# Performance work log

Hardware: AMD Instinct MI355X
Metric: run time of the kernel (lower is better)

Reference implementation:

```python
import jax, jax.numpy as jnp
import numpy as np

N, E, D, G, NTYPES = 50000, 400000, 64, 512, 64


def _bn(x, g, b):
    # BatchNorm1d in training mode: biased batch stats, eps=1e-5, affine g/b
    mu = x.mean(0)
    var = ((x - mu) ** 2).mean(0)
    return g * (x - mu) * jax.lax.rsqrt(var + 1e-5) + b


def _rotmat(a):
    t, p, q = a[0], a[1], a[2]
    ct, st = jnp.cos(t), jnp.sin(t)
    cp, sp = jnp.cos(p), jnp.sin(p)
    cq, sq = jnp.cos(q), jnp.sin(q)
    z = jnp.zeros(())
    o = jnp.ones(())
    Rt = jnp.array([[ct, -st, z], [st, ct, z], [z, z, o]])
    Rp = jnp.array([[cp, z, -sp], [z, o, z], [sp, z, cp]])
    Rq = jnp.array([[o, z, z], [z, cq, -sq], [z, sq, cq]])
    return Rt @ Rp @ Rq


def _egat(src, dst, nf, ef, Wnode, bnode, Wni, Wnj, Wfij, attn, H):
    # DGL EGATConv: edge feats from src/dst node + edge projections, edge-softmax attention over dst
    n = nf.shape[0]
    f_out = jax.nn.leaky_relu((nf @ Wni)[src] + (nf @ Wnj)[dst] + ef @ Wfij)  # [E, H*D]
    f_out = f_out.reshape(-1, H, D)
    e = (f_out * attn[None]).sum(-1)  # [E, H]
    emax = jax.ops.segment_max(e, dst, num_segments=n)
    ee = jnp.exp(e - emax[dst])
    a = ee / jax.ops.segment_sum(ee, dst, num_segments=n)[dst]
    hsrc = (nf @ Wnode + bnode).reshape(n, H, D)[src]
    h_out = jax.ops.segment_sum(hsrc * a[:, :, None], dst, num_segments=n)  # [N, H, D]
    return h_out, f_out


def _layer(src, dst, nh, eh, p, H, last):
    Wnode, bnode, Wni, Wnj, Wfij, attn, bnn_g, bnn_b, bne_g, bne_b, Wpn, bpn, Wpe, bpe = p
    hn, he = _egat(src, dst, nh, eh, Wnode, bnode, Wni, Wnj, Wfij, attn, H)
    if last:
        hn, he = hn.mean(1), he.mean(1)
    else:
        hn, he = hn.reshape(hn.shape[0], -1), he.reshape(he.shape[0], -1)
    hn = _bn(hn, bnn_g, bnn_b)
    he = _bn(he, bne_g, bne_b)
    return hn @ Wpn + bpn + nh, he @ Wpe + bpe + eh


def setup_inputs():
    key = jax.random.key(0)
    kit = iter(jax.random.split(key, 64))

    def rn(shape, s=0.05):
        return jax.random.normal(next(kit), shape, dtype=jnp.float32) * s

    inp = {}
    inp["ntype"] = jax.random.randint(next(kit), (N, 1), 0, NTYPES)
    inp["src"] = jax.random.randint(next(kit), (E,), 0, N)
    inp["dst"] = jax.random.randint(next(kit), (E,), 0, N)
    inp["graph_ids"] = jnp.sort(jax.random.randint(next(kit), (N,), 0, G))
    inp["angles_rot"] = rn((3,), 1.0)
    inp["angles_ref"] = rn((3,), 1.0)
    inp["efeats"] = rn((E, 3), 1.0)
    inp["emb_table"] = rn((NTYPES, D))
    inp["enc_W"] = rn((D, D)); inp["enc_b"] = jnp.zeros((D,))
    inp["ee_W1"] = rn((3, D)); inp["ee_b1"] = jnp.zeros((D,))
    inp["ee_W2"] = rn((D, D)); inp["ee_b2"] = jnp.zeros((D,))
    for nm in ["enc_bn1", "enc_bn2", "ee_bn1", "ee_bn2"]:
        inp[nm + "_g"] = jnp.ones((D,)); inp[nm + "_b"] = jnp.zeros((D,))
    for l, H in [(0, 2), (1, 1)]:
        p = "l%d_" % l
        inp[p + "Wnode"] = rn((D, H * D)); inp[p + "bnode"] = jnp.zeros((H * D,))
        inp[p + "Wni"] = rn((D, H * D)); inp[p + "Wnj"] = rn((D, H * D)); inp[p + "Wfij"] = rn((D, H * D))
        inp[p + "attn"] = rn((H, D))
        inp[p + "bnn_g"] = jnp.ones((H * D,)); inp[p + "bnn_b"] = jnp.zeros((H * D,))
        inp[p + "bne_g"] = jnp.ones((H * D,)); inp[p + "bne_b"] = jnp.zeros((H * D,))
        inp[p + "Wpn"] = rn((H * D, D)); inp[p + "bpn"] = jnp.zeros((D,))
        inp[p + "Wpe"] = rn((H * D, D)); inp[p + "bpe"] = jnp.zeros((D,))
    inp["dec_W"] = rn((4, D, D)); inp["dec_b"] = jnp.zeros((4, D))
    inp["dec_bn_g"] = jnp.ones((4, D)); inp["dec_bn_b"] = jnp.zeros((4, D))
    inp["dec_prelu"] = jnp.full((4,), 0.25, dtype=jnp.float32)
    inp["dec_Wout"] = rn((D, 1)); inp["dec_bout"] = jnp.zeros((1,))
    return inp


def reference(efeats, emb_table, enc_bn1_g, enc_bn1_b, enc_W, enc_b, enc_bn2_g, enc_bn2_b, ee_W1, ee_b1, ee_bn1_g, ee_bn1_b, ee_W2, ee_b2, ee_bn2_g, ee_bn2_b, l0_Wnode, l0_bnode, l0_Wni, l0_Wnj, l0_Wfij, l0_attn, l0_bnn_g, l0_bnn_b, l0_bne_g, l0_bne_b, l0_Wpn, l0_bpn, l0_Wpe, l0_bpe, l1_Wnode, l1_bnode, l1_Wni, l1_Wnj, l1_Wfij, l1_attn, l1_bnn_g, l1_bnn_b, l1_bne_g, l1_bne_b, l1_Wpn, l1_bpn, l1_Wpe, l1_bpe, dec_W, dec_b, dec_bn_g, dec_bn_b, dec_prelu, dec_Wout, dec_bout, ntype, src, dst, graph_ids, angles_rot, angles_ref):
    # node encoder: Embedding -> BN -> ReLU -> Linear -> BN -> ReLU
    nh = emb_table[ntype[:, 0]]
    nh = jax.nn.relu(_bn(nh, enc_bn1_g, enc_bn1_b))
    nh = jax.nn.relu(_bn(nh @ enc_W + enc_b, enc_bn2_g, enc_bn2_b))

    def edge_enc(f):
        h = jax.nn.relu(_bn(f @ ee_W1 + ee_b1, ee_bn1_g, ee_bn1_b))
        return jax.nn.relu(_bn(h @ ee_W2 + ee_b2, ee_bn2_g, ee_bn2_b))

    # rotation matrices built from sampled angles; torch.tensor([...]) detaches -> stop_gradient
    R_rot = jax.lax.stop_gradient(_rotmat(angles_rot))
    R_ref = -jax.lax.stop_gradient(_rotmat(angles_ref))
    eh = edge_enc(efeats @ R_rot) + edge_enc(efeats @ R_ref)

    p0 = (l0_Wnode, l0_bnode, l0_Wni, l0_Wnj, l0_Wfij, l0_attn, l0_bnn_g, l0_bnn_b, l0_bne_g, l0_bne_b, l0_Wpn, l0_bpn, l0_Wpe, l0_bpe)
    p1 = (l1_Wnode, l1_bnode, l1_Wni, l1_Wnj, l1_Wfij, l1_attn, l1_bnn_g, l1_bnn_b, l1_bne_g, l1_bne_b, l1_Wpn, l1_bpn, l1_Wpe, l1_bpe)
    nh, eh = _layer(src, dst, nh, eh, p0, 2, False)
    h1 = nh
    nh, eh = _layer(src, dst, nh, eh, p1, 1, True)
    h2 = nh

    h = nh
    for i in range(4):
        h = _bn(h @ dec_W[i] + dec_b[i], dec_bn_g[i], dec_bn_b[i])
        h = jnp.where(h >= 0.0, h, dec_prelu[i] * h)
    h = h @ dec_Wout + dec_bout
    # dgl.sum_nodes: per-graph sum over batched graphs
    return (h1, h2, jax.ops.segment_sum(h, graph_ids, num_segments=G))
```

## Files before the change

### kernel.cpp

```cpp
#include <hip/hip_runtime.h>
#include <math.h>

#define NN 50000
#define NE 400000
#define NG 512
#define EPS 1e-5f
#define NSLOT 256

typedef unsigned int u32;
typedef unsigned short u16;

typedef __attribute__((ext_vector_type(8))) short s16x8;
typedef __attribute__((ext_vector_type(4))) float f32x4;

__device__ __forceinline__ float b2f(u16 h) { return __uint_as_float(((u32)h) << 16); }
__device__ __forceinline__ u16 f2b(float f) {
    u32 x = __float_as_uint(f);
    u32 r = x + 0x7fffu + ((x >> 16) & 1u);
    return (u16)(r >> 16);
}
struct alignas(16) U16x8 { u16 s[8]; };
struct alignas(8) U16x4 { u16 s[4]; };
struct alignas(4) U16x2 { u16 s[2]; };

__device__ __forceinline__ void f4add(float4& a, const float4 b) {
    a.x += b.x; a.y += b.y; a.z += b.z; a.w += b.w;
}

__device__ __forceinline__ int xcd_swizzle(int orig, int nwg) {
    int xcd = orig & 7;
    int q = nwg >> 3, r = nwg & 7;
    return (xcd < r ? xcd * (q + 1) : r * (q + 1) + (xcd - r) * q) + (orig >> 3);
}

__global__ void setup_kernel(const float* __restrict__ ang_rot, const float* __restrict__ ang_ref,
                             const float* __restrict__ W1, float* __restrict__ RWrot,
                             float* __restrict__ RWref) {
    int c = threadIdx.x;
    for (int which = 0; which < 2; ++which) {
        const float* a = which ? ang_ref : ang_rot;
        float t = a[0], p = a[1], q = a[2];
        float ct = cosf(t), st = sinf(t);
        float cp = cosf(p), sp = sinf(p);
        float cq = cosf(q), sq = sinf(q);
        float Rt[3][3] = {{ct, -st, 0.f}, {st, ct, 0.f}, {0.f, 0.f, 1.f}};
        float Rp[3][3] = {{cp, 0.f, -sp}, {0.f, 1.f, 0.f}, {sp, 0.f, cp}};
        float Rq[3][3] = {{1.f, 0.f, 0.f}, {0.f, cq, -sq}, {0.f, sq, cq}};
        float Rtp[3][3], R[3][3];
        for (int i = 0; i < 3; ++i)
            for (int j = 0; j < 3; ++j) {
                float s = 0.f;
                for (int k = 0; k < 3; ++k) s += Rt[i][k] * Rp[k][j];
                Rtp[i][j] = s;
            }
        for (int i = 0; i < 3; ++i)
            for (int j = 0; j < 3; ++j) {
                float s = 0.f;
                for (int k = 0; k < 3; ++k) s += Rtp[i][k] * Rq[k][j];
                R[i][j] = s;
            }
        float sgn = which ? -1.f : 1.f;
        float* RW = which ? RWref : RWrot;
        if (c < 64) {
            for (int j = 0; j < 3; ++j) {
                float s = 0.f;
                for (int m = 0; m < 3; ++m) s += sgn * R[j][m] * W1[m * 64 + c];
                RW[j * 64 + c] = s;
            }
        }
    }
}

#define NWT 17
struct WtJobs {
    const float* W[NWT];
    u16* WT[NWT];
    int K[NWT];
    int C[NWT];
};
__global__ __launch_bounds__(256) void wt_all_kernel(WtJobs jobs) {
    int job = blockIdx.x >> 5;
    int idx = ((blockIdx.x & 31) << 8) + threadIdx.x;
    int K = jobs.K[job], C = jobs.C[job];
    if (idx >= K * C) return;
    int k = idx / C, c = idx - k * C;
    jobs.WT[job][c * K + k] = f2b(jobs.W[job][idx]);
}

__global__ __launch_bounds__(256) void hist_kernel(const int* __restrict__ dst, int E,
                                                   int* __restrict__ deg) {
    int e = blockIdx.x * 256 + threadIdx.x;
    if (e < E) atomicAdd(&deg[dst[e]], 1);
}

__global__ __launch_bounds__(256) void scan_part_kernel(const int* __restrict__ deg,
                                                        int* __restrict__ bsum, int n) {
    int i = blockIdx.x * 256 + threadIdx.x;
    int v = (i < n) ? deg[i] : 0;
#pragma unroll
    for (int off = 1; off < 64; off <<= 1) v += __shfl_xor(v, off, 64);
    __shared__ int ws[4];
    if ((threadIdx.x & 63) == 0) ws[threadIdx.x >> 6] = v;
    __syncthreads();
    if (threadIdx.x == 0) bsum[blockIdx.x] = ws[0] + ws[1] + ws[2] + ws[3];
}

__global__ __launch_bounds__(256) void scan_top_kernel(int* __restrict__ bsum, int nb,
                                                       int* __restrict__ rowptr, int n,
                                                       int total) {
    __shared__ int s[256];
    int tid = threadIdx.x;
    s[tid] = (tid < nb) ? bsum[tid] : 0;
    __syncthreads();
    for (int off = 1; off < 256; off <<= 1) {
        int v = (tid >= off) ? s[tid - off] : 0;
        __syncthreads();
        s[tid] += v;
        __syncthreads();
    }
    if (tid < nb) bsum[tid] = (tid == 0) ? 0 : s[tid - 1];
    if (tid == 0) rowptr[n] = total;
}

__global__ __launch_bounds__(256) void scan_fill_kernel(const int* __restrict__ deg,
                                                        const int* __restrict__ bsum,
                                                        int* __restrict__ rowptr,
                                                        int* __restrict__ curs, int n) {
    __shared__ int s[256];
    int tid = threadIdx.x;
    int i = blockIdx.x * 256 + tid;
    int v = (i < n) ? deg[i] : 0;
    s[tid] = v;
    __syncthreads();
    for (int off = 1; off < 256; off <<= 1) {
        int t = (tid >= off) ? s[tid - off] : 0;
        __syncthreads();
        s[tid] += t;
        __syncthreads();
    }
    if (i < n) {
        int excl = s[tid] - v + bsum[blockIdx.x];
        rowptr[i] = excl;
        curs[i] = excl;
    }
}

__global__ __launch_bounds__(256) void fill_kernel(const int* __restrict__ src,
                                                   const int* __restrict__ dst,
                                                   const float* __restrict__ ef, int E,
                                                   int* __restrict__ curs,
                                                   int* __restrict__ esrc,
                                                   int* __restrict__ dsts,
                                                   float* __restrict__ efp) {
    int e = blockIdx.x * 256 + threadIdx.x;
    if (e >= E) return;
    int d = dst[e];
    int pos = atomicAdd(&curs[d], 1);
    esrc[pos] = src[e];
    dsts[pos] = d;
    efp[(long)pos * 3 + 0] = ef[(long)e * 3 + 0];
    efp[(long)pos * 3 + 1] = ef[(long)e * 3 + 1];
    efp[(long)pos * 3 + 2] = ef[(long)e * 3 + 2];
}

__global__ __launch_bounds__(256) void gather_emb_kernel(const int* __restrict__ ntype,
                                                         const float* __restrict__ emb,
                                                         u16* __restrict__ out, int n) {
    long i = (long)blockIdx.x * 256 + threadIdx.x;
    long e = i >> 3;
    if (e >= n) return;
    int c0 = (int)(i & 7) * 8;
    int t = ntype[e];
    float4 a = *(const float4*)&emb[(long)t * 64 + c0];
    float4 b = *(const float4*)&emb[(long)t * 64 + c0 + 4];
    U16x8 o;
    o.s[0] = f2b(a.x); o.s[1] = f2b(a.y); o.s[2] = f2b(a.z); o.s[3] = f2b(a.w);
    o.s[4] = f2b(b.x); o.s[5] = f2b(b.y); o.s[6] = f2b(b.z); o.s[7] = f2b(b.w);
    *(U16x8*)&out[e * 64 + c0] = o;
}

__global__ __launch_bounds__(256) void efstats_kernel(const float* __restrict__ ef, int E,
                                                      float* __restrict__ raw) {
    int tid = threadIdx.x;
    float a[9];
#pragma unroll
    for (int j = 0; j < 9; ++j) a[j] = 0.f;
    for (long e = (long)blockIdx.x * 256 + tid; e < E; e += (long)gridDim.x * 256) {
        float f0 = ef[e * 3 + 0], f1 = ef[e * 3 + 1], f2 = ef[e * 3 + 2];
        a[0] += f0; a[1] += f1; a[2] += f2;
        a[3] += f0 * f0; a[4] += f1 * f1; a[5] += f2 * f2;
        a[6] += f0 * f1; a[7] += f0 * f2; a[8] += f1 * f2;
    }
#pragma unroll
    for (int off = 1; off < 64; off <<= 1)
#pragma unroll
        for (int j = 0; j < 9; ++j) a[j] += __shfl_xor(a[j], off, 64);
    __shared__ float sred[4][9];
    int wv = tid >> 6, ln = tid & 63;
    if (ln == 0)
#pragma unroll
        for (int j = 0; j < 9; ++j) sred[wv][j] = a[j];
    __syncthreads();
    if (tid < 9) {
        float v = sred[0][tid] + sred[1][tid] + sred[2][tid] + sred[3][tid];
        atomicAdd(&raw[(size_t)(blockIdx.x & (NSLOT - 1)) * 16 + tid], v);
    }
}

__global__ void ee_stats_kernel(const float* __restrict__ efraw, const float* __restrict__ RWrot,
                                const float* __restrict__ RWref, const float* __restrict__ b1,
                                float* __restrict__ S_rot, float* __restrict__ S_ref, int E) {
    __shared__ float m[9];
    int t = threadIdx.x;
    if (t < 9) {
        float s = 0.f;
        for (int r = 0; r < NSLOT; ++r) s += efraw[r * 16 + t];
        m[t] = s;
    }
    __syncthreads();
    int br = t >> 6, c = t & 63;
    const float* RW = br ? RWref : RWrot;
    float* S = br ? S_ref : S_rot;
    float w0 = RW[c], w1 = RW[64 + c], w2 = RW[128 + c];
    float bb = b1[c];
    float mw = m[0] * w0 + m[1] * w1 + m[2] * w2;
    float sum = mw + (float)E * bb;
    float quad = m[3] * w0 * w0 + m[4] * w1 * w1 + m[5] * w2 * w2 +
                 2.f * (m[6] * w0 * w1 + m[7] * w0 * w2 + m[8] * w1 * w2);
    float ss = quad + 2.f * bb * mw + (float)E * bb * bb;
    S[c] = sum;
    S[64 + c] = ss;
}

template <int COLS>
__global__ __launch_bounds__(256) void colstats_kernel(const u16* __restrict__ xv, int rows,
                                                       float* __restrict__ raw) {
    constexpr int TPR = COLS / 8;
    constexpr int RPB = 256 / TPR;
    __shared__ float4 sA[256], sB[256], sC[256], sD[256];
    int tid = threadIdx.x;
    int c8 = tid % TPR;
    int rl = tid / TPR;
    float s[8], q[8];
#pragma unroll
    for (int j = 0; j < 8; ++j) { s[j] = 0.f; q[j] = 0.f; }
    const long stride = (long)gridDim.x * RPB;
    for (long r = (long)blockIdx.x * RPB + rl; r < rows; r += stride) {
        U16x8 t = *(const U16x8*)&xv[r * COLS + c8 * 8];
#pragma unroll
        for (int j = 0; j < 8; ++j) {
            float v = b2f(t.s[j]);
            s[j] += v;
            q[j] += v * v;
        }
    }
    sA[tid] = make_float4(s[0], s[1], s[2], s[3]);
    sB[tid] = make_float4(s[4], s[5], s[6], s[7]);
    sC[tid] = make_float4(q[0], q[1], q[2], q[3]);
    sD[tid] = make_float4(q[4], q[5], q[6], q[7]);
    __syncthreads();
    for (int off = 128; off >= TPR; off >>= 1) {
        if (tid < off) {
            f4add(sA[tid], sA[tid + off]); f4add(sB[tid], sB[tid + off]);
            f4add(sC[tid], sC[tid + off]); f4add(sD[tid], sD[tid + off]);
        }
        __syncthreads();
    }
    if (tid < TPR) {
        float* slot = raw + (size_t)(blockIdx.x & (NSLOT - 1)) * 256;
        int c = tid * 8;
        float4 a = sA[tid], b = sB[tid], cq = sC[tid], d = sD[tid];
        atomicAdd(&slot[c + 0], a.x); atomicAdd(&slot[c + 1], a.y);
        atomicAdd(&slot[c + 2], a.z); atomicAdd(&slot[c + 3], a.w);
        atomicAdd(&slot[c + 4], b.x); atomicAdd(&slot[c + 5], b.y);
        atomicAdd(&slot[c + 6], b.z); atomicAdd(&slot[c + 7], b.w);
        atomicAdd(&slot[COLS + c + 0], cq.x); atomicAdd(&slot[COLS + c + 1], cq.y);
        atomicAdd(&slot[COLS + c + 2], cq.z); atomicAdd(&slot[COLS + c + 3], cq.w);
        atomicAdd(&slot[COLS + c + 4], d.x); atomicAdd(&slot[COLS + c + 5], d.y);
        atomicAdd(&slot[COLS + c + 6], d.z); atomicAdd(&slot[COLS + c + 7], d.w);
    }
}

__global__ __launch_bounds__(256) void finalize_stats_kernel(const float* __restrict__ raw,
                                                             float* __restrict__ stats, int n) {
    int i = threadIdx.x;
    if (i >= n) return;
    float s = 0.f;
    for (int r = 0; r < NSLOT; ++r) s += raw[r * 256 + i];
    stats[i] = s;
}

__global__ __launch_bounds__(256) void bn_act_kernel(const u16* __restrict__ x,
                                                     u16* __restrict__ y, long rows, int cols,
                                                     const float* __restrict__ acc,
                                                     const float* __restrict__ g,
                                                     const float* __restrict__ b,
                                                     float inv_rows) {
    long i = (long)blockIdx.x * 256 + threadIdx.x;
    long total8 = rows * (long)cols / 8;
    if (i >= total8) return;
    long base = i * 8;
    int c0 = (int)(base % cols);
    U16x8 xv = *(const U16x8*)&x[base];
    U16x8 o;
#pragma unroll
    for (int j = 0; j < 8; ++j) {
        int c = c0 + j;
        float mu = acc[c] * inv_rows;
        float var = acc[cols + c] * inv_rows - mu * mu;
        float al = g[c] * rsqrtf(fmaxf(var, 0.f) + EPS);
        float be = b[c] - mu * al;
        o.s[j] = f2b(fmaxf(al * b2f(xv.s[j]) + be, 0.f));
    }
    *(U16x8*)&y[base] = o;
}


template <int K, int COLS, bool XBF, bool RBF, bool OBF, bool SOUT>
__global__ __launch_bounds__(256) void mfma_mm_kernel(
    const void* __restrict__ Xv, const u16* __restrict__ WT, const float* __restrict__ bias,
    const void* __restrict__ resv, void* __restrict__ Yv, int rows, int preop,
    const float* __restrict__ stats, const float* __restrict__ g, const float* __restrict__ b,
    float inv_rows, const float* __restrict__ prelu, int prelu_idx, float* __restrict__ raw) {
    constexpr int NCT = COLS / 16;
    constexpr int NKK = K / 32;
    __shared__ float al[K], be[K];
    __shared__ float ssum[SOUT ? COLS : 1], ssq[SOUT ? COLS : 1];
    const int tid = threadIdx.x;
    if (preop) {
        for (int k = tid; k < K; k += 256) {
            float mu = stats[k] * inv_rows;
            float var = stats[K + k] * inv_rows - mu * mu;
            float a = g[k] * rsqrtf(fmaxf(var, 0.f) + EPS);
            al[k] = a;
            be[k] = b[k] - mu * a;
        }
    }
    if (SOUT) {
        for (int i = tid; i < COLS; i += 256) { ssum[i] = 0.f; ssq[i] = 0.f; }
    }
    __syncthreads();
    const int lane = tid & 63, wv = tid >> 6;
    const int q = lane >> 4, rr = lane & 15;
    const long r0 = ((long)blockIdx.x * 4 + wv) * 16;
    const bool act = r0 < rows;
    const float pa = (preop == 3) ? prelu[prelu_idx] : 0.f;
    s16x8 afr[NKK];
    if (act) {
#pragma unroll
        for (int kk = 0; kk < NKK; ++kk) {
            float v[8];
            if (XBF) {
                U16x8 t = *(const U16x8*)((const u16*)Xv + (r0 + rr) * K + kk * 32 + q * 8);
#pragma unroll
                for (int j = 0; j < 8; ++j) v[j] = b2f(t.s[j]);
            } else {
                const float* xp = (const float*)Xv + (r0 + rr) * K + kk * 32 + q * 8;
                float4 t0 = *(const float4*)xp;
                float4 t1 = *(const float4*)(xp + 4);
                v[0] = t0.x; v[1] = t0.y; v[2] = t0.z; v[3] = t0.w;
                v[4] = t1.x; v[5] = t1.y; v[6] = t1.z; v[7] = t1.w;
            }
            union { u16 u[8]; s16x8 s; } o;
#pragma unroll
            for (int j = 0; j < 8; ++j) {
                float xx = v[j];
                if (preop) {
                    int k = kk * 32 + q * 8 + j;
                    xx = al[k] * xx + be[k];
                    if (preop == 2) xx = fmaxf(xx, 0.f);
                    else if (preop == 3) xx = (xx >= 0.f) ? xx : pa * xx;
                }
                o.u[j] = f2b(xx);
            }
            afr[kk] = o.s;
        }
#pragma unroll
        for (int ct = 0; ct < NCT; ++ct) {
            f32x4 acc = (f32x4){0.f, 0.f, 0.f, 0.f};
#pragma unroll
            for (int kk = 0; kk < NKK; ++kk) {
                s16x8 bfr = *(const s16x8*)&WT[(size_t)(ct * 16 + rr) * K + kk * 32 + q * 8];
                acc = __builtin_amdgcn_mfma_f32_16x16x32_bf16(afr[kk], bfr, acc, 0, 0, 0);
            }
            int col = ct * 16 + rr;
            float bb = bias ? bias[col] : 0.f;
            float fs = 0.f, fq = 0.f;
#pragma unroll
            for (int r = 0; r < 4; ++r) {
                long orr = r0 + q * 4 + r;
                float vv = acc[r] + bb;
                if (resv) {
                    if (RBF) vv += b2f(((const u16*)resv)[orr * COLS + col]);
                    else vv += ((const float*)resv)[orr * COLS + col];
                }
                if (OBF) ((u16*)Yv)[orr * COLS + col] = f2b(vv);
                else ((float*)Yv)[orr * COLS + col] = vv;
                if (SOUT) { fs += vv; fq += vv * vv; }
            }
            if (SOUT) {
                fs += __shfl_xor(fs, 16, 64); fs += __shfl_xor(fs, 32, 64);
                fq += __shfl_xor(fq, 16, 64); fq += __shfl_xor(fq, 32, 64);
                if (q == 0) {
                    atomicAdd(&ssum[col], fs);
                    atomicAdd(&ssq[col], fq);
                }
            }
        }
    }
    if (SOUT) {
        __syncthreads();
        float* slot = raw + (size_t)(blockIdx.x & (NSLOT - 1)) * 256;
        for (int i = tid; i < COLS; i += 256) {
            atomicAdd(&slot[i], ssum[i]);
            atomicAdd(&slot[COLS + i], ssq[i]);
        }
    }
}

template <int COLS, bool XBF>
__global__ __launch_bounds__(256) void mfma_mm3_kernel(
    const void* __restrict__ Xv, const u16* __restrict__ WT0, const u16* __restrict__ WT1,
    const u16* __restrict__ WT2, const float* __restrict__ bias2, u16* __restrict__ Y0,
    u16* __restrict__ Y1, u16* __restrict__ Y2, int rows) {
    constexpr int NCT = COLS / 16;
    const int tid = threadIdx.x;
    const int lane = tid & 63, wv = tid >> 6;
    const int q = lane >> 4, rr = lane & 15;
    const long r0 = ((long)blockIdx.x * 4 + wv) * 16;
    if (r0 >= rows) return;
    s16x8 afr[2];
#pragma unroll
    for (int kk = 0; kk < 2; ++kk) {
        if (XBF) {
            afr[kk] = *(const s16x8*)((const u16*)Xv + (r0 + rr) * 64 + kk * 32 + q * 8);
        } else {
            const float* xp = (const float*)Xv + (r0 + rr) * 64 + kk * 32 + q * 8;
            float4 t0 = *(const float4*)xp;
            float4 t1 = *(const float4*)(xp + 4);
            union { u16 u[8]; s16x8 s; } o;
            o.u[0] = f2b(t0.x); o.u[1] = f2b(t0.y); o.u[2] = f2b(t0.z); o.u[3] = f2b(t0.w);
            o.u[4] = f2b(t1.x); o.u[5] = f2b(t1.y); o.u[6] = f2b(t1.z); o.u[7] = f2b(t1.w);
            afr[kk] = o.s;
        }
    }
    const u16* wts[3] = {WT0, WT1, WT2};
    u16* ys[3] = {Y0, Y1, Y2};
#pragma unroll
    for (int m = 0; m < 3; ++m) {
#pragma unroll
        for (int ct = 0; ct < NCT; ++ct) {
            f32x4 acc = (f32x4){0.f, 0.f, 0.f, 0.f};
#pragma unroll
            for (int kk = 0; kk < 2; ++kk) {
                s16x8 bfr = *(const s16x8*)&wts[m][(size_t)(ct * 16 + rr) * 64 + kk * 32 + q * 8];
                acc = __builtin_amdgcn_mfma_f32_16x16x32_bf16(afr[kk], bfr, acc, 0, 0, 0);
            }
            int col = ct * 16 + rr;
            float bb = (m == 2) ? bias2[col] : 0.f;
#pragma unroll
            for (int r = 0; r < 4; ++r) {
                long orr = r0 + q * 4 + r;
                ys[m][orr * COLS + col] = f2b(acc[r] + bb);
            }
        }
    }
}

template <bool STORE>
__global__ __launch_bounds__(256) void mfma_ee2_kernel(
    const float* __restrict__ efp, const float* __restrict__ RWrot,
    const float* __restrict__ RWref, const float* __restrict__ b1v, const u16* __restrict__ W2T,
    const float* __restrict__ b2, const float* __restrict__ S1r, const float* __restrict__ S1f,
    const float* __restrict__ S2r, const float* __restrict__ S2f, const float* __restrict__ g1,
    const float* __restrict__ bn1b, const float* __restrict__ g2, const float* __restrict__ bn2b,
    u16* __restrict__ EH, int E, float inv_rows, float* __restrict__ rawA,
    float* __restrict__ rawB) {
    constexpr int ESTR = 72;
    __shared__ float rws[2][192];
    __shared__ float al1[2][64], be1[2][64];
    __shared__ float al2[2][64], be2[2][64];
    __shared__ float ssum[2][64], ssq[2][64];
    __shared__ u16 ets[STORE ? 64 * ESTR : 1];
    const int tid = threadIdx.x;
    if (tid < 192) {
        rws[0][tid] = RWrot[tid];
        rws[1][tid] = RWref[tid];
    }
    if (tid < 128) {
        int br = tid >> 6, k = tid & 63;
        const float* S1 = br ? S1f : S1r;
        float mu = S1[k] * inv_rows;
        float var = S1[64 + k] * inv_rows - mu * mu;
        float a = g1[k] * rsqrtf(fmaxf(var, 0.f) + EPS);
        al1[br][k] = a;
        be1[br][k] = bn1b[k] - mu * a + a * b1v[k];
        if (STORE) {
            const float* S2 = br ? S2f : S2r;
            mu = S2[k] * inv_rows;
            var = S2[64 + k] * inv_rows - mu * mu;
            a = g2[k] * rsqrtf(fmaxf(var, 0.f) + EPS);
            al2[br][k] = a;
            be2[br][k] = bn2b[k] - mu * a + a * b2[k];
        } else {
            ssum[br][k] = 0.f;
            ssq[br][k] = 0.f;
        }
    }
    __syncthreads();
    const int lane = tid & 63, wv = tid >> 6;
    const int q = lane >> 4, rr = lane & 15;
    const long r0 = ((long)blockIdx.x * 4 + wv) * 16;
    const long ar = r0 + rr;
    float e0 = efp[ar * 3], e1 = efp[ar * 3 + 1], e2 = efp[ar * 3 + 2];
    float v0[4][4];
#pragma unroll
    for (int br = 0; br < 2; ++br) {
        s16x8 afr[2];
#pragma unroll
        for (int kk = 0; kk < 2; ++kk) {
            union { u16 u[8]; s16x8 v; } t;
#pragma unroll
            for (int j = 0; j < 8; ++j) {
                int k = kk * 32 + q * 8 + j;
                float tv = e0 * rws[br][k] + e1 * rws[br][64 + k] + e2 * rws[br][128 + k];
                t.u[j] = f2b(fmaxf(al1[br][k] * tv + be1[br][k], 0.f));
            }
            afr[kk] = t.v;
        }
#pragma unroll
        for (int ct = 0; ct < 4; ++ct) {
            f32x4 acc = (f32x4){0.f, 0.f, 0.f, 0.f};
#pragma unroll
            for (int kk = 0; kk < 2; ++kk) {
                s16x8 bfr = *(const s16x8*)&W2T[(size_t)(ct * 16 + rr) * 64 + kk * 32 + q * 8];
                acc = __builtin_amdgcn_mfma_f32_16x16x32_bf16(afr[kk], bfr, acc, 0, 0, 0);
            }
            int col = ct * 16 + rr;
            if (STORE) {
#pragma unroll
                for (int r = 0; r < 4; ++r) {
                    float v = fmaxf(al2[br][col] * acc[r] + be2[br][col], 0.f);
                    if (br == 0) {
                        v0[ct][r] = v;
                    } else {
                        ets[(wv * 16 + q * 4 + r) * ESTR + col] = f2b(v0[ct][r] + v);
                    }
                }
            } else {
                float bb = b2[col];
                float s = 0.f, qq = 0.f;
#pragma unroll
                for (int r = 0; r < 4; ++r) {
                    float v = acc[r] + bb;
                    s += v;
                    qq += v * v;
                }
                s += __shfl_xor(s, 16, 64); s += __shfl_xor(s, 32, 64);
                qq += __shfl_xor(qq, 16, 64); qq += __shfl_xor(qq, 32, 64);
                if (q == 0) {
                    atomicAdd(&ssum[br][col], s);
                    atomicAdd(&ssq[br][col], qq);
                }
            }
        }
    }
    __syncthreads();
    if (STORE) {
        const long rb = (long)blockIdx.x * 64;
        for (int i = tid; i < 64 * 8; i += 256) {
            int row = i >> 3, c8 = i & 7;
            U16x8 v = *(const U16x8*)&ets[row * ESTR + c8 * 8];
            *(U16x8*)&EH[(rb + row) * 64 + c8 * 8] = v;
        }
    } else {
        if (tid < 128) {
            int br = tid >> 6, k = tid & 63;
            float* slot = (br ? rawB : rawA) + (size_t)(blockIdx.x & (NSLOT - 1)) * 256;
            atomicAdd(&slot[k], ssum[br][k]);
            atomicAdd(&slot[64 + k], ssq[br][k]);
        }
    }
}

template <int COLS, bool WRITE_F, bool SOUT>
__global__ __launch_bounds__(256) void mfma_egat_kernel(
    const u16* __restrict__ EH, const u16* __restrict__ WT, const u16* __restrict__ NI,
    const u16* __restrict__ NJ, const int* __restrict__ srcs, const int* __restrict__ dsts,
    const float* __restrict__ attn, u16* __restrict__ Fout, float* __restrict__ eatt, int E,
    float* __restrict__ raw) {
    constexpr int H = COLS / 64;
    constexpr int NCT = COLS / 16;
    constexpr int FSTR = COLS + 8;
    __shared__ float ssum[SOUT ? COLS : 1];
    __shared__ float ssq[SOUT ? COLS : 1];
    __shared__ u16 fts[WRITE_F ? 64 * FSTR : 1];
    const int tid = threadIdx.x;
    if (SOUT) {
        for (int i = tid; i < COLS; i += 256) { ssum[i] = 0.f; ssq[i] = 0.f; }
        __syncthreads();
    }
    const int bid = xcd_swizzle(blockIdx.x, gridDim.x);
    const int lane = tid & 63, wv = tid >> 6;
    const int q = lane >> 4, rr = lane & 15;
    const long r0 = ((long)bid * 4 + wv) * 16;
    s16x8 afr[2];
#pragma unroll
    for (int kk = 0; kk < 2; ++kk)
        afr[kk] = *(const s16x8*)&EH[(r0 + rr) * 64 + kk * 32 + q * 8];
    int sidx[4], didx[4];
#pragma unroll
    for (int r = 0; r < 4; ++r) {
        long orr = r0 + q * 4 + r;
        sidx[r] = srcs[orr];
        didx[r] = dsts[orr];
    }
    f32x4 acc[NCT];
#pragma unroll
    for (int ct = 0; ct < NCT; ++ct) {
        acc[ct] = (f32x4){0.f, 0.f, 0.f, 0.f};
#pragma unroll
        for (int kk = 0; kk < 2; ++kk) {
            s16x8 bfr = *(const s16x8*)&WT[(size_t)(ct * 16 + rr) * 64 + kk * 32 + q * 8];
            acc[ct] = __builtin_amdgcn_mfma_f32_16x16x32_bf16(afr[kk], bfr, acc[ct], 0, 0, 0);
        }
    }
    float part[H][4];
#pragma unroll
    for (int h = 0; h < H; ++h)
#pragma unroll
        for (int r = 0; r < 4; ++r) part[h][r] = 0.f;
#pragma unroll
    for (int ct = 0; ct < NCT; ++ct) {
        int col = ct * 16 + rr;
        float av = attn[col];
        const int h = (H == 2) ? (ct >> 2) : 0;
        float fs = 0.f, fq = 0.f;
#pragma unroll
        for (int r = 0; r < 4; ++r) {
            float f = acc[ct][r] + b2f(NI[(size_t)sidx[r] * COLS + col]) +
                      b2f(NJ[(size_t)didx[r] * COLS + col]);
            f = (f >= 0.f) ? f : 0.01f * f;
            if (WRITE_F) fts[(wv * 16 + q * 4 + r) * FSTR + col] = f2b(f);
            part[h][r] += f * av;
            if (SOUT) { fs += f; fq += f * f; }
        }
        if (SOUT) {
            fs += __shfl_xor(fs, 16, 64); fs += __shfl_xor(fs, 32, 64);
            fq += __shfl_xor(fq, 16, 64); fq += __shfl_xor(fq, 32, 64);
            if (q == 0) {
                atomicAdd(&ssum[col], fs);
                atomicAdd(&ssq[col], fq);
            }
        }
    }
#pragma unroll
    for (int h = 0; h < H; ++h)
#pragma unroll
        for (int r = 0; r < 4; ++r) {
            float p = part[h][r];
            p += __shfl_xor(p, 1, 64);
            p += __shfl_xor(p, 2, 64);
            p += __shfl_xor(p, 4, 64);
            p += __shfl_xor(p, 8, 64);
            part[h][r] = p;
        }
    if (rr == 0) {
#pragma unroll
        for (int r = 0; r < 4; ++r) {
            long pos = r0 + q * 4 + r;
            if (H == 2) {
                eatt[pos * 2 + 0] = part[0][r];
                eatt[pos * 2 + 1] = part[1][r];
            } else {
                eatt[pos] = part[0][r];
            }
        }
    }
    if (WRITE_F) {
        __syncthreads();
        const long rb = (long)bid * 64;
        constexpr int CH = COLS / 8;
        for (int i = tid; i < 64 * CH; i += 256) {
            int row = i / CH, c8 = i % CH;
            U16x8 v = *(const U16x8*)&fts[row * FSTR + c8 * 8];
            *(U16x8*)&Fout[(rb + row) * COLS + c8 * 8] = v;
        }
    }
    if (SOUT) {
        __syncthreads();
        float* slot = raw + (size_t)(blockIdx.x & (NSLOT - 1)) * 256;
        for (int i = tid; i < COLS; i += 256) {
            atomicAdd(&slot[i], ssum[i]);
            atomicAdd(&slot[COLS + i], ssq[i]);
        }
    }
}

__global__ __launch_bounds__(256) void mfma_pe_kernel(
    const u16* __restrict__ X, const u16* __restrict__ WT, const float* __restrict__ bias,
    u16* __restrict__ EHio, int E, const float* __restrict__ stats, const float* __restrict__ g,
    const float* __restrict__ b, float inv_rows) {
    constexpr int ESTR = 72;
    __shared__ float al[128], be[128];
    __shared__ u16 ets[64 * ESTR];
    const int tid = threadIdx.x;
    if (tid < 128) {
        float mu = stats[tid] * inv_rows;
        float var = stats[128 + tid] * inv_rows - mu * mu;
        float a = g[tid] * rsqrtf(fmaxf(var, 0.f) + EPS);
        al[tid] = a;
        be[tid] = b[tid] - mu * a;
    }
    __syncthreads();
    const int lane = tid & 63, wv = tid >> 6;
    const int q = lane >> 4, rr = lane & 15;
    const long r0 = ((long)blockIdx.x * 4 + wv) * 16;
    s16x8 afr[4];
#pragma unroll
    for (int kk = 0; kk < 4; ++kk) {
        U16x8 t = *(const U16x8*)&X[(r0 + rr) * 128 + kk * 32 + q * 8];
        union { u16 u[8]; s16x8 v; } o;
#pragma unroll
        for (int j = 0; j < 8; ++j) {
            int k = kk * 32 + q * 8 + j;
            o.u[j] = f2b(al[k] * b2f(t.s[j]) + be[k]);
        }
        afr[kk] = o.v;
    }
#pragma unroll
    for (int ct = 0; ct < 4; ++ct) {
        f32x4 acc = (f32x4){0.f, 0.f, 0.f, 0.f};
#pragma unroll
        for (int kk = 0; kk < 4; ++kk) {
            s16x8 bfr = *(const s16x8*)&WT[(size_t)(ct * 16 + rr) * 128 + kk * 32 + q * 8];
            acc = __builtin_amdgcn_mfma_f32_16x16x32_bf16(afr[kk], bfr, acc, 0, 0, 0);
        }
        int col = ct * 16 + rr;
        float bb = bias[col];
#pragma unroll
        for (int r = 0; r < 4; ++r)
            ets[(wv * 16 + q * 4 + r) * ESTR + col] = f2b(acc[r] + bb);
    }
    __syncthreads();
    const long rb = (long)blockIdx.x * 64;
#pragma unroll
    for (int g2 = 0; g2 < 2; ++g2) {
        int i = g2 * 256 + tid;
        int row = i >> 3, c8 = i & 7;
        U16x8 st = *(const U16x8*)&ets[row * ESTR + c8 * 8];
        U16x8 old = *(const U16x8*)&EHio[(rb + row) * 64 + c8 * 8];
        U16x8 o;
#pragma unroll
        for (int j = 0; j < 8; ++j) o.s[j] = f2b(b2f(st.s[j]) + b2f(old.s[j]));
        *(U16x8*)&EHio[(rb + row) * 64 + c8 * 8] = o;
    }
}

template <int COLS, bool SOUT>
__global__ __launch_bounds__(256) void csr_aggregate_kernel(
    const int* __restrict__ rowptr, const int* __restrict__ esrc,
    const float* __restrict__ eatt, const u16* __restrict__ nodeh, float* __restrict__ hout,
    int n, float* __restrict__ raw) {
    constexpr int H = COLS / 64;
    constexpr int TPN = COLS / 2;
    constexpr int NPB = 256 / TPN;
    __shared__ float ssum[SOUT ? COLS : 1];
    __shared__ float ssq[SOUT ? COLS : 1];
    int tid = threadIdx.x;
    if (SOUT) {
        for (int i = tid; i < COLS; i += 256) { ssum[i] = 0.f; ssq[i] = 0.f; }
        __syncthreads();
    }
    int node = blockIdx.x * NPB + tid / TPN;
    bool act = node < n;
    int c = (tid % TPN) * 2;
    float a0 = 0.f, a1 = 0.f;
    if (act) {
        int h = (H == 2) ? (c >> 6) : 0;
        int p0 = rowptr[node], p1 = rowptr[node + 1];
        float m = -INFINITY, s = 0.f;
        for (int p = p0; p < p1; ++p) {
            float v = eatt[(long)p * H + h];
            float mn = fmaxf(m, v);
            s = s * expf(m - mn) + expf(v - mn);
            m = mn;
        }
        float inv = (s > 0.f) ? 1.f / s : 0.f;
        for (int p = p0; p < p1; ++p) {
            float w = expf(eatt[(long)p * H + h] - m) * inv;
            U16x2 v = *(const U16x2*)&nodeh[(long)esrc[p] * COLS + c];
            a0 += b2f(v.s[0]) * w;
            a1 += b2f(v.s[1]) * w;
        }
        *(float2*)&hout[(long)node * COLS + c] = make_float2(a0, a1);
    }
    if (SOUT) {
        if (act) {
            atomicAdd(&ssum[c], a0);
            atomicAdd(&ssum[c + 1], a1);
            atomicAdd(&ssq[c], a0 * a0);
            atomicAdd(&ssq[c + 1], a1 * a1);
        }
        __syncthreads();
        float* slot = raw + (size_t)(blockIdx.x & (NSLOT - 1)) * 256;
        for (int i = tid; i < COLS; i += 256) {
            atomicAdd(&slot[i], ssum[i]);
            atomicAdd(&slot[COLS + i], ssq[i]);
        }
    }
}

__global__ __launch_bounds__(256) void decoder_out_kernel(
    const u16* __restrict__ t3, const float* __restrict__ stats, const float* __restrict__ g,
    const float* __restrict__ b, const float* __restrict__ prelu, const float* __restrict__ Wout,
    const float* __restrict__ bout, const int* __restrict__ gid, float* __restrict__ pool,
    int rows, float inv_rows) {
    int tid = threadIdx.x;
    long r = (long)blockIdx.x * 4 + (tid >> 6);
    if (r >= rows) return;
    int k = tid & 63;
    float mu = stats[k] * inv_rows;
    float var = stats[64 + k] * inv_rows - mu * mu;
    float al = g[k] * rsqrtf(fmaxf(var, 0.f) + EPS);
    float be = b[k] - mu * al;
    float a = prelu[3];
    float v = al * b2f(t3[r * 64 + k]) + be;
    v = (v >= 0.f) ? v : a * v;
    v *= Wout[k];
#pragma unroll
    for (int off = 1; off < 64; off <<= 1) v += __shfl_xor(v, off, 64);
    if (k == 0) atomicAdd(&pool[gid[r]], v + bout[0]);
}

extern "C" void kernel_launch(void* const* d_in, const int* in_sizes, int n_in, void* d_out,
                              int out_size, void* d_ws, size_t ws_size, hipStream_t stream) {
    if (n_in < 57) return;
    const int* ntype = (const int*)d_in[0];
    const int* src = (const int*)d_in[1];
    const int* dst = (const int*)d_in[2];
    const int* gid = (const int*)d_in[3];
    const float* ang_rot = (const float*)d_in[4];
    const float* ang_ref = (const float*)d_in[5];
    const float* efeats = (const float*)d_in[6];
    const float* emb = (const float*)d_in[7];
    const float* enc_W = (const float*)d_in[8];
    const float* enc_b = (const float*)d_in[9];
    const float* ee_W1 = (const float*)d_in[10];
    const float* ee_b1 = (const float*)d_in[11];
    const float* ee_W2 = (const float*)d_in[12];
    const float* ee_b2 = (const float*)d_in[13];
    const float* enc_bn1_g = (const float*)d_in[14];
    const float* enc_bn1_b = (const float*)d_in[15];
    const float* enc_bn2_g = (const float*)d_in[16];
    const float* enc_bn2_b = (const float*)d_in[17];
    const float* ee_bn1_g = (const float*)d_in[18];
    const float* ee_bn1_b = (const float*)d_in[19];
    const float* ee_bn2_g = (const float*)d_in[20];
    const float* ee_bn2_b = (const float*)d_in[21];
    const float* l0_Wnode = (const float*)d_in[22];
    const float* l0_bnode = (const float*)d_in[23];
    const float* l0_Wni = (const float*)d_in[24];
    const float* l0_Wnj = (const float*)d_in[25];
    const float* l0_Wfij = (const float*)d_in[26];
    const float* l0_attn = (const float*)d_in[27];
    const float* l0_bnn_g = (const float*)d_in[28];
    const float* l0_bnn_b = (const float*)d_in[29];
    const float* l0_bne_g = (const float*)d_in[30];
    const float* l0_bne_b = (const float*)d_in[31];
    const float* l0_Wpn = (const float*)d_in[32];
    const float* l0_bpn = (const float*)d_in[33];
    const float* l0_Wpe = (const float*)d_in[34];
    const float* l0_bpe = (const float*)d_in[35];
    const float* l1_Wnode = (const float*)d_in[36];
    const float* l1_bnode = (const float*)d_in[37];
    const float* l1_Wni = (const float*)d_in[38];
    const float* l1_Wnj = (const float*)d_in[39];
    const float* l1_Wfij = (const float*)d_in[40];
    const float* l1_attn = (const float*)d_in[41];
    const float* l1_bnn_g = (const float*)d_in[42];
    const float* l1_bnn_b = (const float*)d_in[43];
    const float* l1_Wpn = (const float*)d_in[46];
    const float* l1_bpn = (const float*)d_in[47];
    const float* dec_W = (const float*)d_in[50];
    const float* dec_b = (const float*)d_in[51];
    const float* dec_bn_g = (const float*)d_in[52];
    const float* dec_bn_b = (const float*)d_in[53];
    const float* dec_prelu = (const float*)d_in[54];
    const float* dec_Wout = (const float*)d_in[55];
    const float* dec_bout = (const float*)d_in[56];

    float* out = (float*)d_out;
    float* H1 = out;
    float* H2 = out + (long)NN * 64;
    float* POOL = out + (long)NN * 128;

    char* base = (char*)d_ws;
    size_t off = 0;
    auto alloc = [&](size_t bytes) -> void* {
        off = (off + 255) & ~(size_t)255;
        void* p = base + off;
        off += bytes;
        return p;
    };
    u16* EH = (u16*)alloc((size_t)NE * 64 * 2);
    u16* F128 = (u16*)alloc((size_t)NE * 128 * 2);
    float* EATT = (float*)alloc((size_t)NE * 2 * 4);
    u16* NX = (u16*)alloc((size_t)NN * 64 * 2);
    u16* NI = (u16*)alloc((size_t)NN * 128 * 2);
    u16* NJ = (u16*)alloc((size_t)NN * 128 * 2);
    u16* NHH = (u16*)alloc((size_t)NN * 128 * 2);
    float* HOUT0 = (float*)alloc((size_t)NN * 128 * 4);
    float* HOUT1 = (float*)alloc((size_t)NN * 64 * 4);
    int* ROWPTR = (int*)alloc((size_t)(NN + 1) * 4);
    int* CURS = (int*)alloc((size_t)NN * 4);
    int* ESRC = (int*)alloc((size_t)NE * 4);
    int* DSTS = (int*)alloc((size_t)NE * 4);
    float* EFP = (float*)alloc((size_t)NE * 3 * 4);
    int* BSUM = (int*)alloc((size_t)256 * 4);
    float* RWrot = (float*)alloc(256 * 4);
    float* RWref = (float*)alloc(256 * 4);
    u16* EncWT = (u16*)alloc(4096 * 2);
    u16* W2T = (u16*)alloc(4096 * 2);
    u16* Wni0T = (u16*)alloc(8192 * 2);
    u16* Wnj0T = (u16*)alloc(8192 * 2);
    u16* Wnd0T = (u16*)alloc(8192 * 2);
    u16* WfijT0 = (u16*)alloc(8192 * 2);
    u16* Wpn0T = (u16*)alloc(8192 * 2);
    u16* WpeT = (u16*)alloc(8192 * 2);
    u16* Wni1T = (u16*)alloc(4096 * 2);
    u16* Wnj1T = (u16*)alloc(4096 * 2);
    u16* Wnd1T = (u16*)alloc(4096 * 2);
    u16* WfijT1 = (u16*)alloc(4096 * 2);
    u16* Wpn1T = (u16*)alloc(4096 * 2);
    u16* DecT0 = (u16*)alloc(4096 * 2);
    u16* DecT1 = (u16*)alloc(4096 * 2);
    u16* DecT2 = (u16*)alloc(4096 * 2);
    u16* DecT3 = (u16*)alloc(4096 * 2);
    float* STATS = (float*)alloc((size_t)13 * 256 * 4);
    char* zstart = base + ((off + 255) & ~(size_t)255);
    int* DEG = (int*)alloc((size_t)NN * 4);
    float* STATS_RAW = (float*)alloc((size_t)13 * NSLOT * 256 * 4);
    float* RAWEF = (float*)alloc((size_t)NSLOT * 16 * 4);
    char* zend = base + off;
    if (ws_size < off) return;

    u16* NX0 = F128;
    u16* NT = F128 + (size_t)NN * 64;
    u16* DT0 = NI;
    u16* DT1 = NJ;

    auto RAW = [&](int idx) { return STATS_RAW + (size_t)idx * NSLOT * 256; };
    float* S_enc1 = STATS + 0 * 256;
    float* S_enc2 = STATS + 1 * 256;
    float* S_ee1r = STATS + 2 * 256;
    float* S_ee2r = STATS + 3 * 256;
    float* S_ee1f = STATS + 4 * 256;
    float* S_ee2f = STATS + 5 * 256;
    float* S_bnn0 = STATS + 6 * 256;
    float* S_bne0 = STATS + 7 * 256;
    float* S_bnn1 = STATS + 8 * 256;
    float* S_d0 = STATS + 9 * 256;
    float* S_d1 = STATS + 10 * 256;
    float* S_d2 = STATS + 11 * 256;
    float* S_d3 = STATS + 12 * 256;

    const float invN = 1.f / (float)NN;
    const float invE = 1.f / (float)NE;
    const int GS = 640;
    const int MFB = NE / 64;
    const int NNB = (NN + 63) / 64;
    const int NB = (NN + 255) / 256;

    hipMemsetAsync(zstart, 0, (size_t)(zend - zstart), stream);
    hipMemsetAsync(POOL, 0, (size_t)NG * 4, stream);

    setup_kernel<<<1, 64, 0, stream>>>(ang_rot, ang_ref, ee_W1, RWrot, RWref);
    {
        WtJobs j;
        const float* Ws[NWT] = {enc_W,  ee_W2,  l0_Wni, l0_Wnj, l0_Wnode, l0_Wfij,
                                l0_Wpn, l0_Wpe, l1_Wni, l1_Wnj, l1_Wnode, l1_Wfij,
                                l1_Wpn, dec_W,  dec_W + 4096, dec_W + 8192, dec_W + 12288};
        u16* Ts[NWT] = {EncWT, W2T, Wni0T, Wnj0T, Wnd0T, WfijT0, Wpn0T, WpeT, Wni1T,
                        Wnj1T, Wnd1T, WfijT1, Wpn1T, DecT0, DecT1, DecT2, DecT3};
        int Ks[NWT] = {64, 64, 64, 64, 64, 64, 128, 128, 64, 64, 64, 64, 64, 64, 64, 64, 64};
        int Cs[NWT] = {64, 64, 128, 128, 128, 128, 64, 64, 64, 64, 64, 64, 64, 64, 64, 64, 64};
        for (int i = 0; i < NWT; ++i) { j.W[i] = Ws[i]; j.WT[i] = Ts[i]; j.K[i] = Ks[i]; j.C[i] = Cs[i]; }
        wt_all_kernel<<<NWT * 32, 256, 0, stream>>>(j);
    }

    hist_kernel<<<(NE + 255) / 256, 256, 0, stream>>>(dst, NE, DEG);
    scan_part_kernel<<<NB, 256, 0, stream>>>(DEG, BSUM, NN);
    scan_top_kernel<<<1, 256, 0, stream>>>(BSUM, NB, ROWPTR, NN, NE);
    scan_fill_kernel<<<NB, 256, 0, stream>>>(DEG, BSUM, ROWPTR, CURS, NN);
    fill_kernel<<<(NE + 255) / 256, 256, 0, stream>>>(src, dst, efeats, NE, CURS, ESRC, DSTS,
                                                      EFP);

    gather_emb_kernel<<<(NN * 8 + 255) / 256, 256, 0, stream>>>(ntype, emb, NX0, NN);
    colstats_kernel<64><<<GS, 256, 0, stream>>>(NX0, NN, RAW(0));
    finalize_stats_kernel<<<1, 256, 0, stream>>>(RAW(0), S_enc1, 128);
    mfma_mm_kernel<64, 64, true, false, true, true><<<NNB, 256, 0, stream>>>(
        NX0, EncWT, enc_b, nullptr, NT, NN, 2, S_enc1, enc_bn1_g, enc_bn1_b, invN, nullptr, 0,
        RAW(1));
    finalize_stats_kernel<<<1, 256, 0, stream>>>(RAW(1), S_enc2, 128);
    bn_act_kernel<<<(NN * 8 + 255) / 256, 256, 0, stream>>>(NT, NX, NN, 64, S_enc2, enc_bn2_g,
                                                            enc_bn2_b, invN);

    efstats_kernel<<<256, 256, 0, stream>>>(efeats, NE, RAWEF);
    ee_stats_kernel<<<1, 128, 0, stream>>>(RAWEF, RWrot, RWref, ee_b1, S_ee1r, S_ee1f, NE);
    mfma_ee2_kernel<false><<<MFB, 256, 0, stream>>>(
        EFP, RWrot, RWref, ee_b1, W2T, ee_b2, S_ee1r, S_ee1f, nullptr, nullptr, ee_bn1_g,
        ee_bn1_b, nullptr, nullptr, nullptr, NE, invE, RAW(3), RAW(5));
    finalize_stats_kernel<<<1, 256, 0, stream>>>(RAW(3), S_ee2r, 128);
    finalize_stats_kernel<<<1, 256, 0, stream>>>(RAW(5), S_ee2f, 128);
    mfma_ee2_kernel<true><<<MFB, 256, 0, stream>>>(
        EFP, RWrot, RWref, ee_b1, W2T, ee_b2, S_ee1r, S_ee1f, S_ee2r, S_ee2f, ee_bn1_g, ee_bn1_b,
        ee_bn2_g, ee_bn2_b, EH, NE, invE, nullptr, nullptr);

    mfma_mm3_kernel<128, true><<<NNB, 256, 0, stream>>>(NX, Wni0T, Wnj0T, Wnd0T, l0_bnode, NI,
                                                        NJ, NHH, NN);
    mfma_egat_kernel<128, true, true><<<MFB, 256, 0, stream>>>(
        EH, WfijT0, NI, NJ, ESRC, DSTS, l0_attn, F128, EATT, NE, RAW(7));
    finalize_stats_kernel<<<1, 256, 0, stream>>>(RAW(7), S_bne0, 256);
    csr_aggregate_kernel<128, true><<<(NN + 3) / 4, 256, 0, stream>>>(ROWPTR, ESRC, EATT, NHH,
                                                                      HOUT0, NN, RAW(6));
    finalize_stats_kernel<<<1, 256, 0, stream>>>(RAW(6), S_bnn0, 256);
    mfma_mm_kernel<128, 64, false, true, false, false><<<NNB, 256, 0, stream>>>(
        HOUT0, Wpn0T, l0_bpn, NX, H1, NN, 1, S_bnn0, l0_bnn_g, l0_bnn_b, invN, nullptr, 0,
        nullptr);
    mfma_pe_kernel<<<MFB, 256, 0, stream>>>(F128, WpeT, l0_bpe, EH, NE, S_bne0, l0_bne_g,
                                            l0_bne_b, invE);

    mfma_mm3_kernel<64, false><<<NNB, 256, 0, stream>>>(H1, Wni1T, Wnj1T, Wnd1T, l1_bnode, NI,
                                                        NJ, NHH, NN);
    mfma_egat_kernel<64, false, false><<<MFB, 256, 0, stream>>>(
        EH, WfijT1, NI, NJ, ESRC, DSTS, l1_attn, nullptr, EATT, NE, nullptr);
    csr_aggregate_kernel<64, true><<<(NN + 7) / 8, 256, 0, stream>>>(ROWPTR, ESRC, EATT, NHH,
                                                                     HOUT1, NN, RAW(8));
    finalize_stats_kernel<<<1, 256, 0, stream>>>(RAW(8), S_bnn1, 128);
    mfma_mm_kernel<64, 64, false, false, false, false><<<NNB, 256, 0, stream>>>(
        HOUT1, Wpn1T, l1_bpn, H1, H2, NN, 1, S_bnn1, l1_bnn_g, l1_bnn_b, invN, nullptr, 0,
        nullptr);

    mfma_mm_kernel<64, 64, false, false, true, true><<<NNB, 256, 0, stream>>>(
        H2, DecT0, dec_b, nullptr, DT0, NN, 0, nullptr, nullptr, nullptr, 0.f, nullptr, 0,
        RAW(9));
    finalize_stats_kernel<<<1, 256, 0, stream>>>(RAW(9), S_d0, 128);
    mfma_mm_kernel<64, 64, true, false, true, true><<<NNB, 256, 0, stream>>>(
        DT0, DecT1, dec_b + 64, nullptr, DT1, NN, 3, S_d0, dec_bn_g, dec_bn_b, invN, dec_prelu,
        0, RAW(10));
    finalize_stats_kernel<<<1, 256, 0, stream>>>(RAW(10), S_d1, 128);
    mfma_mm_kernel<64, 64, true, false, true, true><<<NNB, 256, 0, stream>>>(
        DT1, DecT2, dec_b + 128, nullptr, DT0, NN, 3, S_d1, dec_bn_g + 64, dec_bn_b + 64, invN,
        dec_prelu, 1, RAW(11));
    finalize_stats_kernel<<<1, 256, 0, stream>>>(RAW(11), S_d2, 128);
    mfma_mm_kernel<64, 64, true, false, true, true><<<NNB, 256, 0, stream>>>(
        DT0, DecT3, dec_b + 192, nullptr, DT1, NN, 3, S_d2, dec_bn_g + 128, dec_bn_b + 128,
        invN, dec_prelu, 2, RAW(12));
    finalize_stats_kernel<<<1, 256, 0, stream>>>(RAW(12), S_d3, 128);
    decoder_out_kernel<<<(NN + 3) / 4, 256, 0, stream>>>(DT1, S_d3, dec_bn_g + 192,
                                                         dec_bn_b + 192, dec_prelu, dec_Wout,
                                                         dec_bout, gid, POOL, NN, invN);
}
```

Baseline: 864.5 us.

## Fuse embedding column stats into gather, store aggregates in bf16, shrink stat slots

Computes the per-column sum and sum-of-squares for the embedding BN inside the gather kernel using wave shuffles and shared atomics, which removes the separate colstats pass. The CSR aggregation outputs for both layers are now stored as bf16 instead of fp32, and the following matmuls read bf16 input, halving that traffic. NSLOT drops from 256 to 64, so finalize_stats reads fewer partial rows at the cost of more atomic contention per slot. Storing the aggregates in bf16 before BN adds rounding error.

```diff
diff --git a/kernel.cpp b/kernel.cpp
--- a/kernel.cpp
+++ b/kernel.cpp
@@ -5,7 +5,7 @@
 #define NE 400000
 #define NG 512
 #define EPS 1e-5f
-#define NSLOT 256
+#define NSLOT 64
 
 typedef unsigned int u32;
 typedef unsigned short u16;
@@ -165,18 +165,55 @@
 
 __global__ __launch_bounds__(256) void gather_emb_kernel(const int* __restrict__ ntype,
                                                          const float* __restrict__ emb,
-                                                         u16* __restrict__ out, int n) {
-    long i = (long)blockIdx.x * 256 + threadIdx.x;
+                                                         u16* __restrict__ out, int n,
+                                                         float* __restrict__ raw) {
+    __shared__ float ssum[64], ssq[64];
+    int tid = threadIdx.x;
+    if (tid < 64) { ssum[tid] = 0.f; ssq[tid] = 0.f; }
+    __syncthreads();
+    long i = (long)blockIdx.x * 256 + tid;
     long e = i >> 3;
-    if (e >= n) return;
     int c0 = (int)(i & 7) * 8;
-    int t = ntype[e];
-    float4 a = *(const float4*)&emb[(long)t * 64 + c0];
-    float4 b = *(const float4*)&emb[(long)t * 64 + c0 + 4];
-    U16x8 o;
-    o.s[0] = f2b(a.x); o.s[1] = f2b(a.y); o.s[2] = f2b(a.z); o.s[3] = f2b(a.w);
-    o.s[4] = f2b(b.x); o.s[5] = f2b(b.y); o.s[6] = f2b(b.z); o.s[7] = f2b(b.w);
-    *(U16x8*)&out[e * 64 + c0] = o;
+    float v[8];
+    bool act = e < n;
+    if (act) {
+        int t = ntype[e];
+        float4 a = *(const float4*)&emb[(long)t * 64 + c0];
+        float4 b = *(const float4*)&emb[(long)t * 64 + c0 + 4];
+        v[0] = a.x; v[1] = a.y; v[2] = a.z; v[3] = a.w;
+        v[4] = b.x; v[5] = b.y; v[6] = b.z; v[7] = b.w;
+        U16x8 o;
+#pragma unroll
+        for (int j = 0; j < 8; ++j) o.s[j] = f2b(v[j]);
+        *(U16x8*)&out[e * 64 + c0] = o;
+    } else {
+#pragma unroll
+        for (int j = 0; j < 8; ++j) v[j] = 0.f;
+    }
+    float q[8];
+#pragma unroll
+    for (int j = 0; j < 8; ++j) q[j] = v[j] * v[j];
+#pragma unroll
+    for (int off = 8; off < 64; off <<= 1)
+#pragma unroll
+        for (int j = 0; j < 8; ++j) {
+            v[j] += __shfl_xor(v[j], off, 64);
+            q[j] += __shfl_xor(q[j], off, 64);
+        }
+    if ((tid & 63) < 8) {
+        int c = (tid & 7) * 8;
+#pragma unroll
+        for (int j = 0; j < 8; ++j) {
+            atomicAdd(&ssum[c + j], v[j]);
+            atomicAdd(&ssq[c + j], q[j]);
+        }
+    }
+    __syncthreads();
+    if (tid < 64) {
+        float* slot = raw + (size_t)(blockIdx.x & (NSLOT - 1)) * 256;
+        atomicAdd(&slot[tid], ssum[tid]);
+        atomicAdd(&slot[64 + tid], ssq[tid]);
+    }
 }
 
 __global__ __launch_bounds__(256) void efstats_kernel(const float* __restrict__ ef, int E,
@@ -230,55 +267,6 @@
     float ss = quad + 2.f * bb * mw + (float)E * bb * bb;
     S[c] = sum;
     S[64 + c] = ss;
-}
-
-template <int COLS>
-__global__ __launch_bounds__(256) void colstats_kernel(const u16* __restrict__ xv, int rows,
-                                                       float* __restrict__ raw) {
-    constexpr int TPR = COLS / 8;
-    constexpr int RPB = 256 / TPR;
-    __shared__ float4 sA[256], sB[256], sC[256], sD[256];
-    int tid = threadIdx.x;
-    int c8 = tid % TPR;
-    int rl = tid / TPR;
-    float s[8], q[8];
-#pragma unroll
-    for (int j = 0; j < 8; ++j) { s[j] = 0.f; q[j] = 0.f; }
-    const long stride = (long)gridDim.x * RPB;
-    for (long r = (long)blockIdx.x * RPB + rl; r < rows; r += stride) {
-        U16x8 t = *(const U16x8*)&xv[r * COLS + c8 * 8];
-#pragma unroll
-        for (int j = 0; j < 8; ++j) {
-            float v = b2f(t.s[j]);
-            s[j] += v;
-            q[j] += v * v;
-        }
-    }
-    sA[tid] = make_float4(s[0], s[1], s[2], s[3]);
-    sB[tid] = make_float4(s[4], s[5], s[6], s[7]);
-    sC[tid] = make_float4(q[0], q[1], q[2], q[3]);
-    sD[tid] = make_float4(q[4], q[5], q[6], q[7]);
-    __syncthreads();
-    for (int off = 128; off >= TPR; off >>= 1) {
-        if (tid < off) {
-            f4add(sA[tid], sA[tid + off]); f4add(sB[tid], sB[tid + off]);
-            f4add(sC[tid], sC[tid + off]); f4add(sD[tid], sD[tid + off]);
-        }
-        __syncthreads();
-    }
-    if (tid < TPR) {
-        float* slot = raw + (size_t)(blockIdx.x & (NSLOT - 1)) * 256;
-        int c = tid * 8;
-        float4 a = sA[tid], b = sB[tid], cq = sC[tid], d = sD[tid];
-        atomicAdd(&slot[c + 0], a.x); atomicAdd(&slot[c + 1], a.y);
-        atomicAdd(&slot[c + 2], a.z); atomicAdd(&slot[c + 3], a.w);
-        atomicAdd(&slot[c + 4], b.x); atomicAdd(&slot[c + 5], b.y);
-        atomicAdd(&slot[c + 6], b.z); atomicAdd(&slot[c + 7], b.w);
-        atomicAdd(&slot[COLS + c + 0], cq.x); atomicAdd(&slot[COLS + c + 1], cq.y);
-        atomicAdd(&slot[COLS + c + 2], cq.z); atomicAdd(&slot[COLS + c + 3], cq.w);
-        atomicAdd(&slot[COLS + c + 4], d.x); atomicAdd(&slot[COLS + c + 5], d.y);
-        atomicAdd(&slot[COLS + c + 6], d.z); atomicAdd(&slot[COLS + c + 7], d.w);
-    }
 }
 
 __global__ __launch_bounds__(256) void finalize_stats_kernel(const float* __restrict__ raw,
@@ -760,7 +748,7 @@
 template <int COLS, bool SOUT>
 __global__ __launch_bounds__(256) void csr_aggregate_kernel(
     const int* __restrict__ rowptr, const int* __restrict__ esrc,
-    const float* __restrict__ eatt, const u16* __restrict__ nodeh, float* __restrict__ hout,
+    const float* __restrict__ eatt, const u16* __restrict__ nodeh, u16* __restrict__ hout,
     int n, float* __restrict__ raw) {
     constexpr int H = COLS / 64;
     constexpr int TPN = COLS / 2;
@@ -793,7 +781,10 @@
             a0 += b2f(v.s[0]) * w;
             a1 += b2f(v.s[1]) * w;
         }
-        *(float2*)&hout[(long)node * COLS + c] = make_float2(a0, a1);
+        U16x2 o;
+        o.s[0] = f2b(a0);
+        o.s[1] = f2b(a1);
+        *(U16x2*)&hout[(long)node * COLS + c] = o;
     }
     if (SOUT) {
         if (act) {
@@ -910,8 +901,8 @@
     u16* NI = (u16*)alloc((size_t)NN * 128 * 2);
     u16* NJ = (u16*)alloc((size_t)NN * 128 * 2);
     u16* NHH = (u16*)alloc((size_t)NN * 128 * 2);
-    float* HOUT0 = (float*)alloc((size_t)NN * 128 * 4);
-    float* HOUT1 = (float*)alloc((size_t)NN * 64 * 4);
+    u16* HOUT0 = (u16*)alloc((size_t)NN * 128 * 2);
+    u16* HOUT1 = (u16*)alloc((size_t)NN * 64 * 2);
     int* ROWPTR = (int*)alloc((size_t)(NN + 1) * 4);
     int* CURS = (int*)alloc((size_t)NN * 4);
     int* ESRC = (int*)alloc((size_t)NE * 4);
@@ -967,7 +958,6 @@
 
     const float invN = 1.f / (float)NN;
     const float invE = 1.f / (float)NE;
-    const int GS = 640;
     const int MFB = NE / 64;
     const int NNB = (NN + 63) / 64;
     const int NB = (NN + 255) / 256;
@@ -996,8 +986,7 @@
     fill_kernel<<<(NE + 255) / 256, 256, 0, stream>>>(src, dst, efeats, NE, CURS, ESRC, DSTS,
                                                       EFP);
 
-    gather_emb_kernel<<<(NN * 8 + 255) / 256, 256, 0, stream>>>(ntype, emb, NX0, NN);
-    colstats_kernel<64><<<GS, 256, 0, stream>>>(NX0, NN, RAW(0));
+    gather_emb_kernel<<<(NN * 8 + 255) / 256, 256, 0, stream>>>(ntype, emb, NX0, NN, RAW(0));
     finalize_stats_kernel<<<1, 256, 0, stream>>>(RAW(0), S_enc1, 128);
     mfma_mm_kernel<64, 64, true, false, true, true><<<NNB, 256, 0, stream>>>(
         NX0, EncWT, enc_b, nullptr, NT, NN, 2, S_enc1, enc_bn1_g, enc_bn1_b, invN, nullptr, 0,
@@ -1025,7 +1014,7 @@
     csr_aggregate_kernel<128, true><<<(NN + 3) / 4, 256, 0, stream>>>(ROWPTR, ESRC, EATT, NHH,
                                                                       HOUT0, NN, RAW(6));
     finalize_stats_kernel<<<1, 256, 0, stream>>>(RAW(6), S_bnn0, 256);
-    mfma_mm_kernel<128, 64, false, true, false, false><<<NNB, 256, 0, stream>>>(
+    mfma_mm_kernel<128, 64, true, true, false, false><<<NNB, 256, 0, stream>>>(
         HOUT0, Wpn0T, l0_bpn, NX, H1, NN, 1, S_bnn0, l0_bnn_g, l0_bnn_b, invN, nullptr, 0,
         nullptr);
     mfma_pe_kernel<<<MFB, 256, 0, stream>>>(F128, WpeT, l0_bpe, EH, NE, S_bne0, l0_bne_g,
@@ -1038,7 +1027,7 @@
     csr_aggregate_kernel<64, true><<<(NN + 7) / 8, 256, 0, stream>>>(ROWPTR, ESRC, EATT, NHH,
                                                                      HOUT1, NN, RAW(8));
     finalize_stats_kernel<<<1, 256, 0, stream>>>(RAW(8), S_bnn1, 128);
-    mfma_mm_kernel<64, 64, false, false, false, false><<<NNB, 256, 0, stream>>>(
+    mfma_mm_kernel<64, 64, true, false, false, false><<<NNB, 256, 0, stream>>>(
         HOUT1, Wpn1T, l1_bpn, H1, H2, NN, 1, S_bnn1, l1_bnn_g, l1_bnn_b, invN, nullptr, 0,
         nullptr);
 
```

Result: faster. 809.9 us (-6.3%).
